# Kernel tuning notes

Hardware: AMD Instinct MI355X
Metric: run time of the kernel (lower is better)

The kernel has to match this reference:

```python
import jax, jax.numpy as jnp
import numpy as np

IMG, P, CIN, D, NH, NB, NC = 512, 16, 3, 384, 4, 3, 2
HD = D // NH
NP_ = (IMG // P) ** 2
T = NP_ + 1
FF = 4 * D


def _ln(x, s, b, eps=1e-5):
    m = x.mean(-1, keepdims=True)
    v = ((x - m) ** 2).mean(-1, keepdims=True)
    return (x - m) / jnp.sqrt(v + eps) * s + b


def setup_inputs() -> dict:
    key = jax.random.key(0)
    ks = jax.random.split(key, 20)
    s = 0.02
    inp = {
        'x': jax.random.normal(ks[0], (16, CIN, IMG, IMG), jnp.float32),
        'targets': jax.random.randint(ks[1], (16,), 0, NC),
        'conv_w': jax.random.normal(ks[2], (D, CIN, P, P), jnp.float32) * s,
        'conv_b': jnp.zeros((D,), jnp.float32),
        'cls_token': jax.random.normal(ks[3], (1, 1, D), jnp.float32),
        'pos_emb': jax.random.normal(ks[4], (T, D), jnp.float32) * s,
        'ln1_s': jnp.ones((NB, D), jnp.float32), 'ln1_b': jnp.zeros((NB, D), jnp.float32),
        'ln2_s': jnp.ones((NB, D), jnp.float32), 'ln2_b': jnp.zeros((NB, D), jnp.float32),
        'wq': jax.random.normal(ks[5], (NB, D, D), jnp.float32) * s,
        'wk': jax.random.normal(ks[6], (NB, D, D), jnp.float32) * s,
        'wv': jax.random.normal(ks[7], (NB, D, D), jnp.float32) * s,
        'wo': jax.random.normal(ks[8], (NB, D, D), jnp.float32) * s,
        'bo': jnp.zeros((NB, D), jnp.float32),
        'w1': jax.random.normal(ks[9], (NB, D, FF), jnp.float32) * s,
        'b1': jnp.zeros((NB, FF), jnp.float32),
        'w2': jax.random.normal(ks[10], (NB, FF, D), jnp.float32) * s,
        'b2': jnp.zeros((NB, D), jnp.float32),
        'lnf_s': jnp.ones((D,), jnp.float32), 'lnf_b': jnp.zeros((D,), jnp.float32),
        'proj_w': jax.random.normal(ks[11], (D, NC), jnp.float32) * s,
        'proj_b': jnp.zeros((NC,), jnp.float32),
    }
    return inp


def _forward(x, conv_w, conv_b, cls_token, pos_emb, ln1_s, ln1_b, ln2_s, ln2_b,
             wq, wk, wv, wo, bo, w1, b1, w2, b2, lnf_s, lnf_b, proj_w, proj_b):
    B = x.shape[0]
    # patch embedding: conv with kernel==stride == non-overlapping patches
    xp = x.reshape(B, CIN, IMG // P, P, IMG // P, P)
    pe = jnp.einsum('bchpwq,dcpq->bhwd', xp, conv_w).reshape(B, NP_, D) + conv_b
    h = jnp.concatenate([jnp.broadcast_to(cls_token, (B, 1, D)), pe], axis=1)  # (B,T,D)
    h = h + pos_emb
    scale = HD ** (-0.5)
    for i in range(NB):
        hn = _ln(h, ln1_s[i], ln1_b[i])
        q = (hn @ wq[i]).reshape(B, T, NH, HD).transpose(0, 2, 1, 3)
        k = (hn @ wk[i]).reshape(B, T, NH, HD).transpose(0, 2, 1, 3)
        v = (hn @ wv[i]).reshape(B, T, NH, HD).transpose(0, 2, 1, 3)
        # cdist p=2 (Euclidean distance) attention scores
        d2 = (jnp.sum(q * q, -1)[..., :, None] + jnp.sum(k * k, -1)[..., None, :]
              - 2.0 * jnp.einsum('bhqd,bhkd->bhqk', q, k))
        wei = jax.nn.softmax(jnp.sqrt(jnp.maximum(d2, 0.0)) * scale, axis=-1)
        vals = jnp.einsum('bhqk,bhkd->bhqd', wei, v).transpose(0, 2, 1, 3).reshape(B, T, D)
        h = h + vals @ wo[i] + bo[i]
        hn2 = _ln(h, ln2_s[i], ln2_b[i])
        h = h + jax.nn.relu(hn2 @ w1[i] + b1[i]) @ w2[i] + b2[i]
    h = _ln(h, lnf_s, lnf_b)
    logits = h @ proj_w + proj_b
    return logits[:, 0]  # (B, NC) cls-token logits


def reference(x, targets, conv_w, conv_b, cls_token, pos_emb, ln1_s, ln1_b, ln2_s, ln2_b,
              wq, wk, wv, wo, bo, w1, b1, w2, b2, lnf_s, lnf_b, proj_w, proj_b):
    cls_logits = _forward(x, conv_w, conv_b, cls_token, pos_emb, ln1_s, ln1_b, ln2_s, ln2_b,
                          wq, wk, wv, wo, bo, w1, b1, w2, b2, lnf_s, lnf_b, proj_w, proj_b)
    logp = jax.nn.log_softmax(cls_logits, axis=-1)
    loss = -jnp.mean(jnp.take_along_axis(logp, targets[:, None], axis=1))
    return (cls_logits, loss)
```

## Files before the change

kernel.cpp:

```cpp
#include <hip/hip_runtime.h>
#include <math.h>


#define BATCH   16
#define TSEQ    1025
#define DMODEL  384
#define NHEAD   4
#define HDIM    96
#define NBLK    3
#define FFDIM   1536
#define IMGSZ   512
#define NPATCHI 1024
#define MROWS   (BATCH*TSEQ)
#define MPATCH  (BATCH*NPATCHI)
#define KPE     768
#define ATT_SCALE 0.10206207261596577f

typedef __attribute__((ext_vector_type(8))) __bf16 bf16x8;
typedef __attribute__((ext_vector_type(4))) float  f32x4;

__device__ __forceinline__ f32x4 fzero4() {
  f32x4 v; v[0] = 0.f; v[1] = 0.f; v[2] = 0.f; v[3] = 0.f; return v;
}
__device__ __forceinline__ bf16x8 bzero8() {
  bf16x8 v;
#pragma unroll
  for (int j = 0; j < 8; ++j) v[j] = (__bf16)0.f;
  return v;
}

template<int EPI>
__global__ __launch_bounds__(256, 2) void mgemm_k(
    const __bf16* __restrict__ A, const __bf16* __restrict__ Bt,
    const float* __restrict__ bias, const float* __restrict__ res,
    float* __restrict__ Cf, __bf16* __restrict__ Cb, int M, int N, int K)
{
  __shared__ __bf16 Al[2][128][40];
  __shared__ __bf16 Bl[2][128][40];
  const int tid = threadIdx.x;
  const int lane = tid & 63;
  const int w = tid >> 6;
  const int wr = w >> 1, wc = w & 1;
  const int l15 = lane & 15, g = lane >> 4;
  const int row0 = blockIdx.x * 128, col0 = blockIdx.y * 128;
  const int srow = tid >> 1, soff = (tid & 1) * 16;
  int ar = row0 + srow; if (ar > M - 1) ar = M - 1;
  const __bf16* ap = A + (size_t)ar * K + soff;
  const __bf16* bp = Bt + (size_t)(col0 + srow) * K + soff;

  f32x4 acc[4][4];
#pragma unroll
  for (int i = 0; i < 4; ++i)
#pragma unroll
    for (int j = 0; j < 4; ++j) acc[i][j] = fzero4();

  const int nk = K >> 5;
  bf16x8 ra0 = *(const bf16x8*)ap;
  bf16x8 ra1 = *(const bf16x8*)(ap + 8);
  bf16x8 rb0 = *(const bf16x8*)bp;
  bf16x8 rb1 = *(const bf16x8*)(bp + 8);
  *(bf16x8*)&Al[0][srow][soff]     = ra0;
  *(bf16x8*)&Al[0][srow][soff + 8] = ra1;
  *(bf16x8*)&Bl[0][srow][soff]     = rb0;
  *(bf16x8*)&Bl[0][srow][soff + 8] = rb1;
  __syncthreads();
  int cur = 0;
  for (int kt = 0; kt < nk; ++kt) {
    const bool pf = (kt + 1 < nk);
    if (pf) {
      const __bf16* a2 = ap + (size_t)(kt + 1) * 32;
      const __bf16* b2 = bp + (size_t)(kt + 1) * 32;
      ra0 = *(const bf16x8*)a2; ra1 = *(const bf16x8*)(a2 + 8);
      rb0 = *(const bf16x8*)b2; rb1 = *(const bf16x8*)(b2 + 8);
    }
    bf16x8 af[4], bfr[4];
#pragma unroll
    for (int mi = 0; mi < 4; ++mi)
      af[mi] = *(const bf16x8*)&Al[cur][wr * 64 + mi * 16 + l15][g * 8];
#pragma unroll
    for (int ni = 0; ni < 4; ++ni)
      bfr[ni] = *(const bf16x8*)&Bl[cur][wc * 64 + ni * 16 + l15][g * 8];
#pragma unroll
    for (int mi = 0; mi < 4; ++mi)
#pragma unroll
      for (int ni = 0; ni < 4; ++ni)
        acc[mi][ni] = __builtin_amdgcn_mfma_f32_16x16x32_bf16(
            af[mi], bfr[ni], acc[mi][ni], 0, 0, 0);
    if (pf) {
      *(bf16x8*)&Al[cur ^ 1][srow][soff]     = ra0;
      *(bf16x8*)&Al[cur ^ 1][srow][soff + 8] = ra1;
      *(bf16x8*)&Bl[cur ^ 1][srow][soff]     = rb0;
      *(bf16x8*)&Bl[cur ^ 1][srow][soff + 8] = rb1;
    }
    __syncthreads();
    cur ^= 1;
  }
#pragma unroll
  for (int ni = 0; ni < 4; ++ni) {
    const int gc = col0 + wc * 64 + ni * 16 + l15;
    const float bv = (EPI & 1) ? bias[gc] : 0.f;
#pragma unroll
    for (int mi = 0; mi < 4; ++mi) {
#pragma unroll
      for (int r = 0; r < 4; ++r) {
        const int gr = row0 + wr * 64 + mi * 16 + g * 4 + r;
        if (gr >= M) continue;
        float v = acc[mi][ni][r] + bv;
        if (EPI & 2) v = fmaxf(v, 0.f);
        if (EPI & 4) v += res[(size_t)gr * N + gc];
        if (EPI & 8)  Cf[(size_t)gr * N + gc] = v;
        if (EPI & 16) Cb[(size_t)gr * N + gc] = (__bf16)v;
      }
    }
  }
}

__global__ __launch_bounds__(256, 2) void attn_k(
    const __bf16* __restrict__ qkv, const float* __restrict__ sq2,
    const float* __restrict__ sk2, __bf16* __restrict__ O)
{
  __shared__ __bf16 Kl[64][104];
  __shared__ __bf16 Vt[96][72];
  __shared__ __bf16 Pl[128][72];
  const int qt = blockIdx.x, bh = blockIdx.y;
  const int bb = bh >> 2, hh = bh & 3;
  const int tid = threadIdx.x;
  const int w = tid >> 6, lane = tid & 63;
  const int l15 = lane & 15, g = lane >> 4;
  const int q0 = qt * 128 + w * 32;
  const float* sq2h = sq2 + (size_t)bh * TSEQ;
  const float* sk2h = sk2 + (size_t)bh * TSEQ;

  bf16x8 qf[2][3];
  float sqv[2][4];
#pragma unroll
  for (int m = 0; m < 2; ++m) {
    int qr = q0 + m * 16 + l15; if (qr > TSEQ - 1) qr = TSEQ - 1;
    const __bf16* qp = qkv + (size_t)(bb * TSEQ + qr) * 1152 + hh * 96 + g * 8;
#pragma unroll
    for (int kf = 0; kf < 3; ++kf) qf[m][kf] = *(const bf16x8*)(qp + kf * 32);
#pragma unroll
    for (int r = 0; r < 4; ++r) {
      int qq = q0 + m * 16 + g * 4 + r; if (qq > TSEQ - 1) qq = TSEQ - 1;
      sqv[m][r] = sq2h[qq];
    }
  }

  float mrun[2][4], lrun[2][4];
  f32x4 accO[2][6];
#pragma unroll
  for (int m = 0; m < 2; ++m)
#pragma unroll
    for (int r = 0; r < 4; ++r) { mrun[m][r] = -INFINITY; lrun[m][r] = 0.f; }
#pragma unroll
  for (int m = 0; m < 2; ++m)
#pragma unroll
    for (int n = 0; n < 6; ++n) accO[m][n] = fzero4();

  for (int kt2 = 0; kt2 < 17; ++kt2) {
    const int kbase = kt2 * 64;
    bf16x8 kr[3], vr[3];
#pragma unroll
    for (int i = 0; i < 3; ++i) {
      const int c = tid + i * 256;
      const int row = c / 12, cc = c - row * 12;
      const int kg = kbase + row;
      if (kg < TSEQ) {
        const __bf16* kp = qkv + (size_t)(bb * TSEQ + kg) * 1152 + 384 + hh * 96 + cc * 8;
        kr[i] = *(const bf16x8*)kp;
        vr[i] = *(const bf16x8*)(kp + 384);
      } else { kr[i] = bzero8(); vr[i] = bzero8(); }
    }
#pragma unroll
    for (int i = 0; i < 3; ++i) {
      const int c = tid + i * 256;
      const int row = c / 12, cc = c - row * 12;
      *(bf16x8*)&Kl[row][cc * 8] = kr[i];
#pragma unroll
      for (int j = 0; j < 8; ++j) Vt[cc * 8 + j][row] = vr[i][j];
    }
    __syncthreads();

    f32x4 sf[2][4];
#pragma unroll
    for (int m = 0; m < 2; ++m)
#pragma unroll
      for (int ks = 0; ks < 4; ++ks) sf[m][ks] = fzero4();
#pragma unroll
    for (int ks = 0; ks < 4; ++ks) {
      bf16x8 kb0 = *(const bf16x8*)&Kl[ks * 16 + l15][g * 8];
      bf16x8 kb1 = *(const bf16x8*)&Kl[ks * 16 + l15][32 + g * 8];
      bf16x8 kb2 = *(const bf16x8*)&Kl[ks * 16 + l15][64 + g * 8];
#pragma unroll
      for (int m = 0; m < 2; ++m) {
        sf[m][ks] = __builtin_amdgcn_mfma_f32_16x16x32_bf16(qf[m][0], kb0, sf[m][ks], 0, 0, 0);
        sf[m][ks] = __builtin_amdgcn_mfma_f32_16x16x32_bf16(qf[m][1], kb1, sf[m][ks], 0, 0, 0);
        sf[m][ks] = __builtin_amdgcn_mfma_f32_16x16x32_bf16(qf[m][2], kb2, sf[m][ks], 0, 0, 0);
      }
    }

    float nmax[2][4];
#pragma unroll
    for (int m = 0; m < 2; ++m)
#pragma unroll
      for (int r = 0; r < 4; ++r) nmax[m][r] = -INFINITY;
#pragma unroll
    for (int ks = 0; ks < 4; ++ks) {
      const int kgl = kbase + ks * 16 + l15;
      const bool kvld = (kgl < TSEQ);
      const float kv2 = kvld ? sk2h[kvld ? kgl : 0] : 0.f;
#pragma unroll
      for (int m = 0; m < 2; ++m)
#pragma unroll
        for (int r = 0; r < 4; ++r) {
          const float d2 = sqv[m][r] + kv2 - 2.f * sf[m][ks][r];
          const float s = kvld ? sqrtf(fmaxf(d2, 0.f)) * ATT_SCALE : -INFINITY;
          sf[m][ks][r] = s;
          nmax[m][r] = fmaxf(nmax[m][r], s);
        }
    }
#pragma unroll
    for (int m = 0; m < 2; ++m)
#pragma unroll
      for (int r = 0; r < 4; ++r) {
        float v = nmax[m][r];
        v = fmaxf(v, __shfl_xor(v, 1, 64));
        v = fmaxf(v, __shfl_xor(v, 2, 64));
        v = fmaxf(v, __shfl_xor(v, 4, 64));
        v = fmaxf(v, __shfl_xor(v, 8, 64));
        const float mn = fmaxf(mrun[m][r], v);
        const float f = __expf(mrun[m][r] - mn);
        mrun[m][r] = mn;
        lrun[m][r] *= f;
#pragma unroll
        for (int n = 0; n < 6; ++n) accO[m][n][r] *= f;
      }
    float ps[2][4] = {{0.f, 0.f, 0.f, 0.f}, {0.f, 0.f, 0.f, 0.f}};
#pragma unroll
    for (int ks = 0; ks < 4; ++ks)
#pragma unroll
      for (int m = 0; m < 2; ++m)
#pragma unroll
        for (int r = 0; r < 4; ++r) {
          const float p = __expf(sf[m][ks][r] - mrun[m][r]);
          ps[m][r] += p;
          Pl[w * 32 + m * 16 + g * 4 + r][ks * 16 + l15] = (__bf16)p;
        }
#pragma unroll
    for (int m = 0; m < 2; ++m)
#pragma unroll
      for (int r = 0; r < 4; ++r) {
        float v = ps[m][r];
        v += __shfl_xor(v, 1, 64);
        v += __shfl_xor(v, 2, 64);
        v += __shfl_xor(v, 4, 64);
        v += __shfl_xor(v, 8, 64);
        lrun[m][r] += v;
      }

#pragma unroll
    for (int ks2 = 0; ks2 < 2; ++ks2) {
      bf16x8 pa[2];
#pragma unroll
      for (int m = 0; m < 2; ++m)
        pa[m] = *(const bf16x8*)&Pl[w * 32 + m * 16 + l15][ks2 * 32 + g * 8];
#pragma unroll
      for (int n = 0; n < 6; ++n) {
        bf16x8 vb = *(const bf16x8*)&Vt[n * 16 + l15][ks2 * 32 + g * 8];
#pragma unroll
        for (int m = 0; m < 2; ++m)
          accO[m][n] = __builtin_amdgcn_mfma_f32_16x16x32_bf16(pa[m], vb, accO[m][n], 0, 0, 0);
      }
    }
    __syncthreads();
  }

#pragma unroll
  for (int m = 0; m < 2; ++m)
#pragma unroll
    for (int r = 0; r < 4; ++r) {
      const int qr = q0 + m * 16 + g * 4 + r;
      if (qr >= TSEQ) continue;
      const float inv = 1.f / lrun[m][r];
#pragma unroll
      for (int n = 0; n < 6; ++n)
        O[(size_t)(bb * TSEQ + qr) * 384 + hh * 96 + n * 16 + l15] =
            (__bf16)(accO[m][n][r] * inv);
    }
}

__global__ __launch_bounds__(256) void im2col_k(
    const float* __restrict__ x, __bf16* __restrict__ Ai)
{
  const int i = blockIdx.x * 256 + threadIdx.x;
  const int row = i / 96;
  const int k = (i - row * 96) * 8;
  const int b = row >> 10;
  const int pidx = row & 1023;
  const int py = pidx >> 5, px = pidx & 31;
  const int cc = k >> 8;
  const int rem = k & 255;
  const int p = rem >> 4, q = rem & 15;
  const float* src = x + ((size_t)((b * 3 + cc) * IMGSZ + py * 16 + p)) * IMGSZ
                       + px * 16 + q;
  const float4 a = *(const float4*)src;
  const float4 c4 = *(const float4*)(src + 4);
  bf16x8 o;
  o[0] = (__bf16)a.x;  o[1] = (__bf16)a.y;  o[2] = (__bf16)a.z;  o[3] = (__bf16)a.w;
  o[4] = (__bf16)c4.x; o[5] = (__bf16)c4.y; o[6] = (__bf16)c4.z; o[7] = (__bf16)c4.w;
  *(bf16x8*)&Ai[(size_t)i * 8] = o;
}

__global__ void wt_k(const float* __restrict__ src, size_t srcZ,
                     __bf16* __restrict__ dst, size_t dstZ, int K, int N)
{
  __shared__ float t[32][33];
  const float* s = src + blockIdx.z * srcZ;
  __bf16* d = dst + blockIdx.z * dstZ;
  const int k0 = blockIdx.x * 32, n0 = blockIdx.y * 32;
  const int tx = threadIdx.x, ty = threadIdx.y;
#pragma unroll
  for (int i = 0; i < 4; ++i)
    t[ty + 8 * i][tx] = s[(size_t)(k0 + ty + 8 * i) * N + n0 + tx];
  __syncthreads();
#pragma unroll
  for (int i = 0; i < 4; ++i)
    d[(size_t)(n0 + ty + 8 * i) * K + k0 + tx] = (__bf16)t[tx][ty + 8 * i];
}

__global__ void cvt_k(const float* __restrict__ src, __bf16* __restrict__ dst, int n8)
{
  const int i = blockIdx.x * 256 + threadIdx.x;
  if (i >= n8) return;
  const float4 a = *(const float4*)&src[(size_t)i * 8];
  const float4 b = *(const float4*)&src[(size_t)i * 8 + 4];
  bf16x8 o;
  o[0] = (__bf16)a.x; o[1] = (__bf16)a.y; o[2] = (__bf16)a.z; o[3] = (__bf16)a.w;
  o[4] = (__bf16)b.x; o[5] = (__bf16)b.y; o[6] = (__bf16)b.z; o[7] = (__bf16)b.w;
  *(bf16x8*)&dst[(size_t)i * 8] = o;
}

__global__ __launch_bounds__(256) void embed_k(
    const float* __restrict__ pe, const float* __restrict__ cls,
    const float* __restrict__ pos, float* __restrict__ h)
{
  const int i = blockIdx.x * 256 + threadIdx.x;
  const int row = i / 96;
  const int d4 = (i - row * 96) * 4;
  const int b = row / TSEQ;
  const int t = row - b * TSEQ;
  const float4 po = *(const float4*)&pos[(size_t)t * DMODEL + d4];
  float4 r;
  if (t == 0) {
    const float4 cv = *(const float4*)&cls[d4];
    r = make_float4(cv.x + po.x, cv.y + po.y, cv.z + po.z, cv.w + po.w);
  } else {
    const float4 pv = *(const float4*)&pe[((size_t)(b * NPATCHI + t - 1)) * DMODEL + d4];
    r = make_float4(pv.x + po.x, pv.y + po.y, pv.z + po.z, pv.w + po.w);
  }
  *(float4*)&h[(size_t)row * DMODEL + d4] = r;
}

__global__ __launch_bounds__(256) void ln_k(
    const float* __restrict__ in, const float* __restrict__ sc,
    const float* __restrict__ bi, __bf16* __restrict__ out)
{
  const int w = threadIdx.x >> 6, lane = threadIdx.x & 63;
  const int row = blockIdx.x * 4 + w;
  const float* r = in + (size_t)row * DMODEL;
  float v[6], sum = 0.f, ss = 0.f;
#pragma unroll
  for (int j = 0; j < 6; ++j) {
    const float xv = r[lane + 64 * j];
    v[j] = xv; sum += xv; ss += xv * xv;
  }
#pragma unroll
  for (int m = 1; m < 64; m <<= 1) {
    sum += __shfl_xor(sum, m, 64);
    ss  += __shfl_xor(ss,  m, 64);
  }
  const float mean = sum * (1.f / 384.f);
  const float var  = ss * (1.f / 384.f) - mean * mean;
  const float rstd = rsqrtf(var + 1e-5f);
  __bf16* o = out + (size_t)row * DMODEL;
#pragma unroll
  for (int j = 0; j < 6; ++j) {
    const int col = lane + 64 * j;
    o[col] = (__bf16)((v[j] - mean) * rstd * sc[col] + bi[col]);
  }
}

__global__ __launch_bounds__(256) void sumsq_k(
    const __bf16* __restrict__ qkv, float* __restrict__ sq2,
    float* __restrict__ sk2)
{
  const int w = threadIdx.x >> 6, lane = threadIdx.x & 63;
  const int row = blockIdx.x * 4 + w;
  const int h = lane >> 4, lg = lane & 15;
  const __bf16* q = qkv + (size_t)row * 1152 + h * HDIM;
  float s1 = 0.f, s2 = 0.f;
#pragma unroll
  for (int j = 0; j < 6; ++j) {
    const float a = (float)q[lg + 16 * j];
    const float c = (float)q[384 + lg + 16 * j];
    s1 += a * a; s2 += c * c;
  }
#pragma unroll
  for (int m = 1; m < 16; m <<= 1) {
    s1 += __shfl_xor(s1, m, 64);
    s2 += __shfl_xor(s2, m, 64);
  }
  if (lg == 0) {
    const int b = row / TSEQ, t = row - b * TSEQ;
    sq2[((size_t)b * NHEAD + h) * TSEQ + t] = s1;
    sk2[((size_t)b * NHEAD + h) * TSEQ + t] = s2;
  }
}

__global__ __launch_bounds__(256) void head_k(
    const float* __restrict__ h, const float* __restrict__ gs,
    const float* __restrict__ gb, const float* __restrict__ pw,
    const float* __restrict__ pb, const int* __restrict__ tgt,
    float* __restrict__ out)
{
  __shared__ float lg[BATCH][2];
  const int w = threadIdx.x >> 6, lane = threadIdx.x & 63;
  for (int b = w; b < BATCH; b += 4) {
    const float* r = h + (size_t)b * TSEQ * DMODEL;
    float v[6], sum = 0.f, ss = 0.f;
#pragma unroll
    for (int j = 0; j < 6; ++j) {
      const float xv = r[lane + 64 * j];
      v[j] = xv; sum += xv; ss += xv * xv;
    }
#pragma unroll
    for (int m = 1; m < 64; m <<= 1) {
      sum += __shfl_xor(sum, m, 64);
      ss  += __shfl_xor(ss,  m, 64);
    }
    const float mean = sum * (1.f / 384.f);
    const float var  = ss * (1.f / 384.f) - mean * mean;
    const float rstd = rsqrtf(var + 1e-5f);
    float l0 = 0.f, l1 = 0.f;
#pragma unroll
    for (int j = 0; j < 6; ++j) {
      const int col = lane + 64 * j;
      const float hnv = (v[j] - mean) * rstd * gs[col] + gb[col];
      l0 = fmaf(hnv, pw[col * 2 + 0], l0);
      l1 = fmaf(hnv, pw[col * 2 + 1], l1);
    }
#pragma unroll
    for (int m = 1; m < 64; m <<= 1) {
      l0 += __shfl_xor(l0, m, 64);
      l1 += __shfl_xor(l1, m, 64);
    }
    if (lane == 0) { lg[b][0] = l0 + pb[0]; lg[b][1] = l1 + pb[1]; }
  }
  __syncthreads();
  if (threadIdx.x < 32)
    out[threadIdx.x] = lg[threadIdx.x >> 1][threadIdx.x & 1];
  if (threadIdx.x == 0) {
    float acc = 0.f;
    for (int b = 0; b < BATCH; ++b) {
      const float a = lg[b][0], c = lg[b][1];
      const float mx = fmaxf(a, c);
      const float lse = mx + logf(expf(a - mx) + expf(c - mx));
      const float lp = ((tgt[b] == 0) ? a : c) - lse;
      acc += lp;
    }
    out[32] = -acc * (1.f / BATCH);
  }
}

extern "C" void kernel_launch(void* const* d_in, const int* in_sizes, int n_in,
                              void* d_out, int out_size, void* d_ws, size_t ws_size,
                              hipStream_t stream)
{
  const float* x       = (const float*)d_in[0];
  const int*   targets = (const int*)  d_in[1];
  const float* conv_w  = (const float*)d_in[2];
  const float* conv_b  = (const float*)d_in[3];
  const float* cls_tok = (const float*)d_in[4];
  const float* pos_emb = (const float*)d_in[5];
  const float* ln1_s   = (const float*)d_in[6];
  const float* ln1_b   = (const float*)d_in[7];
  const float* ln2_s   = (const float*)d_in[8];
  const float* ln2_b   = (const float*)d_in[9];
  const float* wq      = (const float*)d_in[10];
  const float* wk      = (const float*)d_in[11];
  const float* wv      = (const float*)d_in[12];
  const float* wo      = (const float*)d_in[13];
  const float* bo      = (const float*)d_in[14];
  const float* w1      = (const float*)d_in[15];
  const float* b1      = (const float*)d_in[16];
  const float* w2      = (const float*)d_in[17];
  const float* b2      = (const float*)d_in[18];
  const float* lnf_s   = (const float*)d_in[19];
  const float* lnf_b   = (const float*)d_in[20];
  const float* proj_w  = (const float*)d_in[21];
  const float* proj_b  = (const float*)d_in[22];

  char* p = (char*)d_ws;
  auto alloc = [&](size_t bytes) -> void* {
    void* r = (void*)p; p += (bytes + 255) & ~(size_t)255; return r;
  };
  float*  h     = (float*) alloc((size_t)MROWS * DMODEL * 4);
  __bf16* hn    = (__bf16*)alloc((size_t)MROWS * DMODEL * 2);
  __bf16* qkv   = (__bf16*)alloc((size_t)MROWS * 1152 * 2);
  __bf16* Obuf  = (__bf16*)alloc((size_t)MROWS * DMODEL * 2);
  float*  pe    = (float*) alloc((size_t)MPATCH * DMODEL * 4);
  float*  sq2   = (float*) alloc((size_t)BATCH * NHEAD * TSEQ * 4);
  float*  sk2   = (float*) alloc((size_t)BATCH * NHEAD * TSEQ * 4);
  __bf16* cwb   = (__bf16*)alloc((size_t)DMODEL * KPE * 2);
  __bf16* wqkvT = (__bf16*)alloc((size_t)NBLK * 1152 * DMODEL * 2);
  __bf16* woT   = (__bf16*)alloc((size_t)NBLK * DMODEL * DMODEL * 2);
  __bf16* w1T   = (__bf16*)alloc((size_t)NBLK * FFDIM * DMODEL * 2);
  __bf16* w2T   = (__bf16*)alloc((size_t)NBLK * DMODEL * FFDIM * 2);
  if ((size_t)(p - (char*)d_ws) > ws_size) return;
  __bf16* Ai  = qkv;
  __bf16* ffb = qkv;

  cvt_k<<<144, 256, 0, stream>>>(conv_w, cwb, (DMODEL * KPE) / 8);
  {
    dim3 blk(32, 8);
    wt_k<<<dim3(12, 12, 3), blk, 0, stream>>>(wq, (size_t)DMODEL * DMODEL,
        wqkvT + 0,               (size_t)1152 * DMODEL, DMODEL, DMODEL);
    wt_k<<<dim3(12, 12, 3), blk, 0, stream>>>(wk, (size_t)DMODEL * DMODEL,
        wqkvT + 384 * DMODEL,    (size_t)1152 * DMODEL, DMODEL, DMODEL);
    wt_k<<<dim3(12, 12, 3), blk, 0, stream>>>(wv, (size_t)DMODEL * DMODEL,
        wqkvT + 768 * DMODEL,    (size_t)1152 * DMODEL, DMODEL, DMODEL);
    wt_k<<<dim3(12, 12, 3), blk, 0, stream>>>(wo, (size_t)DMODEL * DMODEL,
        woT, (size_t)DMODEL * DMODEL, DMODEL, DMODEL);
    wt_k<<<dim3(12, 48, 3), blk, 0, stream>>>(w1, (size_t)DMODEL * FFDIM,
        w1T, (size_t)FFDIM * DMODEL, DMODEL, FFDIM);
    wt_k<<<dim3(48, 12, 3), blk, 0, stream>>>(w2, (size_t)FFDIM * DMODEL,
        w2T, (size_t)DMODEL * FFDIM, FFDIM, DMODEL);
  }

  im2col_k<<<6144, 256, 0, stream>>>(x, Ai);
  mgemm_k<9><<<dim3(128, 3), 256, 0, stream>>>(
      Ai, cwb, conv_b, nullptr, pe, nullptr, MPATCH, DMODEL, KPE);
  embed_k<<<6150, 256, 0, stream>>>(pe, cls_tok, pos_emb, h);

  for (int i = 0; i < NBLK; ++i) {
    ln_k<<<4100, 256, 0, stream>>>(h, ln1_s + i * DMODEL, ln1_b + i * DMODEL, hn);
    mgemm_k<16><<<dim3(129, 9), 256, 0, stream>>>(
        hn, wqkvT + (size_t)i * 1152 * DMODEL, nullptr, nullptr,
        nullptr, qkv, MROWS, 1152, DMODEL);
    sumsq_k<<<4100, 256, 0, stream>>>(qkv, sq2, sk2);
    attn_k<<<dim3(9, BATCH * NHEAD), 256, 0, stream>>>(qkv, sq2, sk2, Obuf);
    mgemm_k<13><<<dim3(129, 3), 256, 0, stream>>>(
        Obuf, woT + (size_t)i * DMODEL * DMODEL, bo + i * DMODEL, h,
        h, nullptr, MROWS, DMODEL, DMODEL);
    ln_k<<<4100, 256, 0, stream>>>(h, ln2_s + i * DMODEL, ln2_b + i * DMODEL, hn);
    mgemm_k<19><<<dim3(129, 12), 256, 0, stream>>>(
        hn, w1T + (size_t)i * FFDIM * DMODEL, b1 + i * FFDIM, nullptr,
        nullptr, ffb, MROWS, FFDIM, DMODEL);
    mgemm_k<13><<<dim3(129, 3), 256, 0, stream>>>(
        ffb, w2T + (size_t)i * DMODEL * FFDIM, b2 + i * DMODEL, h,
        h, nullptr, MROWS, DMODEL, FFDIM);
  }

  head_k<<<1, 256, 0, stream>>>(h, lnf_s, lnf_b, proj_w, proj_b, targets,
                                (float*)d_out);
}
```

Baseline: 1.351 ms.

## Pre-transpose V globally, halve attention query tile, prefetch next KV chunk

Adds a separate kernel that writes V for each head transposed and padded into a global buffer, so attention loads V rows with vector stores into shared memory. Before, each chunk did a scalar element-by-element transpose in LDS. The attention kernel now gives each wave 16 query rows instead of 32, which doubles the grid to 17x64 blocks and allows occupancy 4. The next K/V chunk is loaded into registers while the current one is computed, and s_setprio wraps the MFMA sections. The costs are an extra kernel launch and global round trip for V, plus K tiles reread by twice as many blocks.

```diff
diff --git a/kernel.cpp b/kernel.cpp
--- a/kernel.cpp
+++ b/kernel.cpp
@@ -14,6 +14,7 @@
 #define MROWS   (BATCH*TSEQ)
 #define MPATCH  (BATCH*NPATCHI)
 #define KPE     768
+#define VTS     1088
 #define ATT_SCALE 0.10206207261596577f
 
 typedef __attribute__((ext_vector_type(8))) __bf16 bf16x8;
@@ -115,178 +116,184 @@
   }
 }
 
-__global__ __launch_bounds__(256, 2) void attn_k(
-    const __bf16* __restrict__ qkv, const float* __restrict__ sq2,
-    const float* __restrict__ sk2, __bf16* __restrict__ O)
+__global__ void vtr_k(const __bf16* __restrict__ qkv, __bf16* __restrict__ Vt)
+{
+  __shared__ __bf16 t[32][33];
+  const int bh = blockIdx.z;
+  const int bb = bh >> 2, hh = bh & 3;
+  const int t0 = blockIdx.x * 32;
+  const int d0 = blockIdx.y * 32;
+  const int tx = threadIdx.x, ty = threadIdx.y;
+#pragma unroll
+  for (int i = 0; i < 4; ++i) {
+    const int tt = t0 + ty + 8 * i;
+    t[ty + 8 * i][tx] = (tt < TSEQ)
+        ? qkv[(size_t)(bb * TSEQ + tt) * 1152 + 768 + hh * 96 + d0 + tx]
+        : (__bf16)0.f;
+  }
+  __syncthreads();
+#pragma unroll
+  for (int i = 0; i < 4; ++i)
+    Vt[((size_t)bh * 96 + d0 + ty + 8 * i) * VTS + t0 + tx] = t[tx][ty + 8 * i];
+}
+
+__global__ __launch_bounds__(256, 4) void attn_k(
+    const __bf16* __restrict__ qkv, const __bf16* __restrict__ Vtg,
+    const float* __restrict__ sq2, const float* __restrict__ sk2,
+    __bf16* __restrict__ O)
 {
   __shared__ __bf16 Kl[64][104];
-  __shared__ __bf16 Vt[96][72];
-  __shared__ __bf16 Pl[128][72];
+  __shared__ __bf16 Vl[96][72];
+  __shared__ __bf16 Pl[64][72];
   const int qt = blockIdx.x, bh = blockIdx.y;
   const int bb = bh >> 2, hh = bh & 3;
   const int tid = threadIdx.x;
   const int w = tid >> 6, lane = tid & 63;
   const int l15 = lane & 15, g = lane >> 4;
-  const int q0 = qt * 128 + w * 32;
+  const int q0 = qt * 64 + w * 16;
   const float* sq2h = sq2 + (size_t)bh * TSEQ;
   const float* sk2h = sk2 + (size_t)bh * TSEQ;
-
-  bf16x8 qf[2][3];
-  float sqv[2][4];
-#pragma unroll
-  for (int m = 0; m < 2; ++m) {
-    int qr = q0 + m * 16 + l15; if (qr > TSEQ - 1) qr = TSEQ - 1;
+  const __bf16* vbase = Vtg + (size_t)bh * 96 * VTS;
+
+  bf16x8 qf[3];
+  float sqv[4];
+  {
+    int qr = q0 + l15; if (qr > TSEQ - 1) qr = TSEQ - 1;
     const __bf16* qp = qkv + (size_t)(bb * TSEQ + qr) * 1152 + hh * 96 + g * 8;
 #pragma unroll
-    for (int kf = 0; kf < 3; ++kf) qf[m][kf] = *(const bf16x8*)(qp + kf * 32);
+    for (int kf = 0; kf < 3; ++kf) qf[kf] = *(const bf16x8*)(qp + kf * 32);
 #pragma unroll
     for (int r = 0; r < 4; ++r) {
-      int qq = q0 + m * 16 + g * 4 + r; if (qq > TSEQ - 1) qq = TSEQ - 1;
-      sqv[m][r] = sq2h[qq];
-    }
-  }
-
-  float mrun[2][4], lrun[2][4];
-  f32x4 accO[2][6];
-#pragma unroll
-  for (int m = 0; m < 2; ++m)
-#pragma unroll
-    for (int r = 0; r < 4; ++r) { mrun[m][r] = -INFINITY; lrun[m][r] = 0.f; }
-#pragma unroll
-  for (int m = 0; m < 2; ++m)
-#pragma unroll
-    for (int n = 0; n < 6; ++n) accO[m][n] = fzero4();
-
-  for (int kt2 = 0; kt2 < 17; ++kt2) {
-    const int kbase = kt2 * 64;
-    bf16x8 kr[3], vr[3];
+      int qq = q0 + g * 4 + r; if (qq > TSEQ - 1) qq = TSEQ - 1;
+      sqv[r] = sq2h[qq];
+    }
+  }
+
+  float mrun[4], lrun[4];
+  f32x4 accO[6];
+#pragma unroll
+  for (int r = 0; r < 4; ++r) { mrun[r] = -INFINITY; lrun[r] = 0.f; }
+#pragma unroll
+  for (int n = 0; n < 6; ++n) accO[n] = fzero4();
+
+  bf16x8 kr[3], vr[3];
+  auto load_chunk = [&](int c) {
+    const int kbase = c * 64;
 #pragma unroll
     for (int i = 0; i < 3; ++i) {
-      const int c = tid + i * 256;
-      const int row = c / 12, cc = c - row * 12;
+      const int idx = tid + i * 256;
+      const int row = idx / 12, cc = idx - row * 12;
       const int kg = kbase + row;
-      if (kg < TSEQ) {
-        const __bf16* kp = qkv + (size_t)(bb * TSEQ + kg) * 1152 + 384 + hh * 96 + cc * 8;
-        kr[i] = *(const bf16x8*)kp;
-        vr[i] = *(const bf16x8*)(kp + 384);
-      } else { kr[i] = bzero8(); vr[i] = bzero8(); }
-    }
+      kr[i] = (kg < TSEQ)
+          ? *(const bf16x8*)(qkv + (size_t)(bb * TSEQ + kg) * 1152 + 384
+                             + hh * 96 + cc * 8)
+          : bzero8();
+      const int d = idx >> 3, o8 = (idx & 7) * 8;
+      vr[i] = *(const bf16x8*)(vbase + (size_t)d * VTS + kbase + o8);
+    }
+  };
+
+  load_chunk(0);
+
+  for (int c = 0; c < 17; ++c) {
+    const int kbase = c * 64;
+    __syncthreads();
 #pragma unroll
     for (int i = 0; i < 3; ++i) {
-      const int c = tid + i * 256;
-      const int row = c / 12, cc = c - row * 12;
+      const int idx = tid + i * 256;
+      const int row = idx / 12, cc = idx - row * 12;
       *(bf16x8*)&Kl[row][cc * 8] = kr[i];
-#pragma unroll
-      for (int j = 0; j < 8; ++j) Vt[cc * 8 + j][row] = vr[i][j];
+      const int d = idx >> 3, o8 = (idx & 7) * 8;
+      *(bf16x8*)&Vl[d][o8] = vr[i];
     }
     __syncthreads();
-
-    f32x4 sf[2][4];
-#pragma unroll
-    for (int m = 0; m < 2; ++m)
-#pragma unroll
-      for (int ks = 0; ks < 4; ++ks) sf[m][ks] = fzero4();
+    if (c + 1 < 17) load_chunk(c + 1);
+
+    f32x4 sf[4];
+#pragma unroll
+    for (int ks = 0; ks < 4; ++ks) sf[ks] = fzero4();
+    __builtin_amdgcn_s_setprio(1);
 #pragma unroll
     for (int ks = 0; ks < 4; ++ks) {
       bf16x8 kb0 = *(const bf16x8*)&Kl[ks * 16 + l15][g * 8];
       bf16x8 kb1 = *(const bf16x8*)&Kl[ks * 16 + l15][32 + g * 8];
       bf16x8 kb2 = *(const bf16x8*)&Kl[ks * 16 + l15][64 + g * 8];
-#pragma unroll
-      for (int m = 0; m < 2; ++m) {
-        sf[m][ks] = __builtin_amdgcn_mfma_f32_16x16x32_bf16(qf[m][0], kb0, sf[m][ks], 0, 0, 0);
-        sf[m][ks] = __builtin_amdgcn_mfma_f32_16x16x32_bf16(qf[m][1], kb1, sf[m][ks], 0, 0, 0);
-        sf[m][ks] = __builtin_amdgcn_mfma_f32_16x16x32_bf16(qf[m][2], kb2, sf[m][ks], 0, 0, 0);
-      }
-    }
-
-    float nmax[2][4];
-#pragma unroll
-    for (int m = 0; m < 2; ++m)
-#pragma unroll
-      for (int r = 0; r < 4; ++r) nmax[m][r] = -INFINITY;
+      sf[ks] = __builtin_amdgcn_mfma_f32_16x16x32_bf16(qf[0], kb0, sf[ks], 0, 0, 0);
+      sf[ks] = __builtin_amdgcn_mfma_f32_16x16x32_bf16(qf[1], kb1, sf[ks], 0, 0, 0);
+      sf[ks] = __builtin_amdgcn_mfma_f32_16x16x32_bf16(qf[2], kb2, sf[ks], 0, 0, 0);
+    }
+    __builtin_amdgcn_s_setprio(0);
+
+    float nmax[4] = {-INFINITY, -INFINITY, -INFINITY, -INFINITY};
 #pragma unroll
     for (int ks = 0; ks < 4; ++ks) {
       const int kgl = kbase + ks * 16 + l15;
       const bool kvld = (kgl < TSEQ);
-      const float kv2 = kvld ? sk2h[kvld ? kgl : 0] : 0.f;
-#pragma unroll
-      for (int m = 0; m < 2; ++m)
-#pragma unroll
-        for (int r = 0; r < 4; ++r) {
-          const float d2 = sqv[m][r] + kv2 - 2.f * sf[m][ks][r];
-          const float s = kvld ? sqrtf(fmaxf(d2, 0.f)) * ATT_SCALE : -INFINITY;
-          sf[m][ks][r] = s;
-          nmax[m][r] = fmaxf(nmax[m][r], s);
-        }
-    }
-#pragma unroll
-    for (int m = 0; m < 2; ++m)
+      const float kv2 = sk2h[kvld ? kgl : 0];
 #pragma unroll
       for (int r = 0; r < 4; ++r) {
-        float v = nmax[m][r];
-        v = fmaxf(v, __shfl_xor(v, 1, 64));
-        v = fmaxf(v, __shfl_xor(v, 2, 64));
-        v = fmaxf(v, __shfl_xor(v, 4, 64));
-        v = fmaxf(v, __shfl_xor(v, 8, 64));
-        const float mn = fmaxf(mrun[m][r], v);
-        const float f = __expf(mrun[m][r] - mn);
-        mrun[m][r] = mn;
-        lrun[m][r] *= f;
-#pragma unroll
-        for (int n = 0; n < 6; ++n) accO[m][n][r] *= f;
+        const float d2 = sqv[r] + kv2 - 2.f * sf[ks][r];
+        const float s = kvld ? sqrtf(fmaxf(d2, 0.f)) * ATT_SCALE : -INFINITY;
+        sf[ks][r] = s;
+        nmax[r] = fmaxf(nmax[r], s);
       }
-    float ps[2][4] = {{0.f, 0.f, 0.f, 0.f}, {0.f, 0.f, 0.f, 0.f}};
+    }
+#pragma unroll
+    for (int r = 0; r < 4; ++r) {
+      float v = nmax[r];
+      v = fmaxf(v, __shfl_xor(v, 1, 64));
+      v = fmaxf(v, __shfl_xor(v, 2, 64));
+      v = fmaxf(v, __shfl_xor(v, 4, 64));
+      v = fmaxf(v, __shfl_xor(v, 8, 64));
+      const float mn = fmaxf(mrun[r], v);
+      const float f = __expf(mrun[r] - mn);
+      mrun[r] = mn;
+      lrun[r] *= f;
+#pragma unroll
+      for (int n = 0; n < 6; ++n) accO[n][r] *= f;
+    }
+    float ps[4] = {0.f, 0.f, 0.f, 0.f};
 #pragma unroll
     for (int ks = 0; ks < 4; ++ks)
 #pragma unroll
-      for (int m = 0; m < 2; ++m)
-#pragma unroll
-        for (int r = 0; r < 4; ++r) {
-          const float p = __expf(sf[m][ks][r] - mrun[m][r]);
-          ps[m][r] += p;
-          Pl[w * 32 + m * 16 + g * 4 + r][ks * 16 + l15] = (__bf16)p;
-        }
-#pragma unroll
-    for (int m = 0; m < 2; ++m)
-#pragma unroll
       for (int r = 0; r < 4; ++r) {
-        float v = ps[m][r];
-        v += __shfl_xor(v, 1, 64);
-        v += __shfl_xor(v, 2, 64);
-        v += __shfl_xor(v, 4, 64);
-        v += __shfl_xor(v, 8, 64);
-        lrun[m][r] += v;
+        const float p = __expf(sf[ks][r] - mrun[r]);
+        ps[r] += p;
+        Pl[w * 16 + g * 4 + r][ks * 16 + l15] = (__bf16)p;
       }
-
+#pragma unroll
+    for (int r = 0; r < 4; ++r) {
+      float v = ps[r];
+      v += __shfl_xor(v, 1, 64);
+      v += __shfl_xor(v, 2, 64);
+      v += __shfl_xor(v, 4, 64);
+      v += __shfl_xor(v, 8, 64);
+      lrun[r] += v;
+    }
+
+    __builtin_amdgcn_s_setprio(1);
 #pragma unroll
     for (int ks2 = 0; ks2 < 2; ++ks2) {
-      bf16x8 pa[2];
-#pragma unroll
-      for (int m = 0; m < 2; ++m)
-        pa[m] = *(const bf16x8*)&Pl[w * 32 + m * 16 + l15][ks2 * 32 + g * 8];
+      bf16x8 pa = *(const bf16x8*)&Pl[w * 16 + l15][ks2 * 32 + g * 8];
 #pragma unroll
       for (int n = 0; n < 6; ++n) {
-        bf16x8 vb = *(const bf16x8*)&Vt[n * 16 + l15][ks2 * 32 + g * 8];
-#pragma unroll
-        for (int m = 0; m < 2; ++m)
-          accO[m][n] = __builtin_amdgcn_mfma_f32_16x16x32_bf16(pa[m], vb, accO[m][n], 0, 0, 0);
+        bf16x8 vb = *(const bf16x8*)&Vl[n * 16 + l15][ks2 * 32 + g * 8];
+        accO[n] = __builtin_amdgcn_mfma_f32_16x16x32_bf16(pa, vb, accO[n], 0, 0, 0);
       }
     }
-    __syncthreads();
-  }
-
-#pragma unroll
-  for (int m = 0; m < 2; ++m)
-#pragma unroll
-    for (int r = 0; r < 4; ++r) {
-      const int qr = q0 + m * 16 + g * 4 + r;
-      if (qr >= TSEQ) continue;
-      const float inv = 1.f / lrun[m][r];
-#pragma unroll
-      for (int n = 0; n < 6; ++n)
-        O[(size_t)(bb * TSEQ + qr) * 384 + hh * 96 + n * 16 + l15] =
-            (__bf16)(accO[m][n][r] * inv);
-    }
+    __builtin_amdgcn_s_setprio(0);
+  }
+
+#pragma unroll
+  for (int r = 0; r < 4; ++r) {
+    const int qr = q0 + g * 4 + r;
+    if (qr >= TSEQ) continue;
+    const float inv = 1.f / lrun[r];
+#pragma unroll
+    for (int n = 0; n < 6; ++n)
+      O[(size_t)(bb * TSEQ + qr) * 384 + hh * 96 + n * 16 + l15] =
+          (__bf16)(accO[n][r] * inv);
+  }
 }
 
 __global__ __launch_bounds__(256) void im2col_k(
@@ -519,6 +526,7 @@
   if ((size_t)(p - (char*)d_ws) > ws_size) return;
   __bf16* Ai  = qkv;
   __bf16* ffb = qkv;
+  __bf16* Vtg = (__bf16*)pe;
 
   cvt_k<<<144, 256, 0, stream>>>(conv_w, cwb, (DMODEL * KPE) / 8);
   {
@@ -548,7 +556,8 @@
         hn, wqkvT + (size_t)i * 1152 * DMODEL, nullptr, nullptr,
         nullptr, qkv, MROWS, 1152, DMODEL);
     sumsq_k<<<4100, 256, 0, stream>>>(qkv, sq2, sk2);
-    attn_k<<<dim3(9, BATCH * NHEAD), 256, 0, stream>>>(qkv, sq2, sk2, Obuf);
+    vtr_k<<<dim3(34, 3, 64), dim3(32, 8), 0, stream>>>(qkv, Vtg);
+    attn_k<<<dim3(17, 64), 256, 0, stream>>>(qkv, Vtg, sq2, sk2, Obuf);
     mgemm_k<13><<<dim3(129, 3), 256, 0, stream>>>(
         Obuf, woT + (size_t)i * DMODEL * DMODEL, bo + i * DMODEL, h,
         h, nullptr, MROWS, DMODEL, DMODEL);
```

Result: faster. 1.296 ms (-4.0%).
